# Kernel tuning notes

Hardware: AMD Instinct MI355X
Metric: run time of the kernel (lower is better)

Reference implementation:

```python
import jax, jax.numpy as jnp
import numpy as np

CX, CY, FX, FY = 334.081, 169.808, 460.585, 460.268
EPS = 1e-07
T_ITER = 1000
MIN_POINTS = 5000
H, W, B = 360, 640, 2


def _point_cloud(depth_img):
    # depth_img: [C,H,W]; channel 2 if C==3 else channel 0
    depth = depth_img[2] if depth_img.shape[0] == 3 else depth_img[0]
    rows, cols = depth.shape
    c = jnp.arange(cols, dtype=depth.dtype)[None, :]
    r = jnp.arange(rows, dtype=depth.dtype)[:, None]
    valid = (depth > 0) & (depth < 65535)
    nanv = jnp.float32(jnp.nan)
    z = jnp.where(valid, depth / 1000.0, nanv)
    x = jnp.where(valid, z * (c - CX) / FX, nanv)
    y = jnp.where(valid, z * (r - CY) / FY, nanv)
    pcd = jnp.stack([x.ravel(), y.ravel(), z.ravel()], axis=1)  # [N,3]
    return pcd, valid.ravel()


def setup_inputs() -> dict:
    key = jax.random.key(0)
    k1, k2 = jax.random.split(key)
    fake = jax.random.uniform(k1, (B, 1, H, W), dtype=jnp.float32)
    real = jax.random.uniform(k2, (B, 1, H, W), dtype=jnp.float32)
    return {"fake": fake, "real": real, "epoch": 5, "show_image": 0}


def _forward(fake, real, epoch):
    real_pcd, vr = _point_cloud(real[0])
    fake_pcd, vf = _point_cloud(fake[0])
    real_pcd = real_pcd * 1000.0
    fake_pcd = fake_pcd * 1000.0
    # pcd[pcd==0] = eps  (NaN==0 is False, NaNs preserved)
    real_pcd = jnp.where(real_pcd == 0, EPS, real_pcd)
    fake_pcd = jnp.where(fake_pcd == 0, EPS, fake_pcd)

    # combined validity mask (real-valid then fake-valid filtering chain)
    m = vr & vf
    cnt = jnp.maximum(jnp.sum(m), 1)

    def sel(v, fill):
        return jnp.where(m, v, fill)

    def mrmse(a, b):
        d = sel(a, 0.0) - sel(b, 0.0)
        return jnp.sqrt(jnp.sum(d * d) / cnt)

    lossX = mrmse(real_pcd[:, 0], fake_pcd[:, 0])
    lossY = mrmse(real_pcd[:, 1], fake_pcd[:, 1])
    lossZ = mrmse(real_pcd[:, 2], fake_pcd[:, 2])
    dlog = jnp.log(jnp.abs(sel(real_pcd[:, 2], 1.0))) - jnp.log(jnp.abs(sel(fake_pcd[:, 2], 1.0)))
    RMSE_log = 10000.0 * jnp.sqrt(jnp.sum(jnp.where(m, dlog * dlog, 0.0)) / cnt)
    loss17 = RMSE_log * jnp.abs(10.0 * (3.0 - jnp.exp(lossX) - jnp.exp(lossY) - jnp.exp(lossZ)))

    # ---- batched RANSAC plane fit on normalized fake cloud ----
    nan_cloud = jnp.where(jnp.isnan(fake_pcd), 0.0, fake_pcd)
    pts = nan_cloud / jnp.max(nan_cloud)  # [N,3]
    N = pts.shape[0]
    thresh = jnp.maximum(jnp.float32(0.025 - 0.001 * epoch), jnp.float32(0.005))

    rkey = jax.random.key(42)
    idx = jax.random.randint(rkey, (T_ITER, 3), 0, N)  # 3 sample points per trial
    p = pts[idx]  # [T,3,3]
    vA = p[:, 1] - p[:, 0]
    vB = p[:, 2] - p[:, 0]
    nrm = jnp.cross(vA, vB)
    nrm = nrm / jnp.linalg.norm(nrm, axis=1, keepdims=True)  # unit normals [T,3]
    kk = -jnp.sum(nrm * p[:, 1], axis=1)  # plane offsets [T]
    dist = pts @ nrm.T + kk[None, :]  # [N,T], |n|=1 so no extra divide
    inl = jnp.abs(dist) <= thresh  # [N,T]
    counts = jnp.sum(inl, axis=0)  # [T]
    # keep first trial with strictly-largest count among counts > minPoints
    score = jnp.where(counts > MIN_POINTS, counts, -1)
    best = jnp.argmax(score)
    a, b, c, d = nrm[best, 0], nrm[best, 1], nrm[best, 2], kk[best]
    inlier_mask = inl[:, best]  # [N]

    # translation/rotation were built via torch.tensor(...) -> detached in torch
    trans = jax.lax.stop_gradient(jnp.stack([jnp.zeros(()), jnp.zeros(()), d / c]))
    n2 = a * a + b * b + c * c
    cos_t = c / jnp.sqrt(n2)
    sin_t = jnp.sqrt((a * a + b * b) / n2)
    sab = jnp.sqrt(a * a + b * b)
    u1 = b / sab
    u2 = -a / sab
    R = jnp.stack([
        jnp.stack([cos_t + u1 * u1 * (1 - cos_t), u1 * u2 * (1 - cos_t), u2 * sin_t]),
        jnp.stack([u1 * u2 * (1 - cos_t), cos_t + u2 * u2 * (1 - cos_t), -u1 * sin_t]),
        jnp.stack([-u2 * sin_t, u1 * sin_t, cos_t]),
    ])
    Rt = jax.lax.stop_gradient(R).T  # torch transposes before matmul

    plane_pts = pts + trans
    zc = (plane_pts @ Rt)[:, 2]  # rotated z for all points; inliers selected by mask
    icnt = jnp.maximum(jnp.sum(inlier_mask), 1)
    zmax = jnp.max(jnp.where(inlier_mask, zc, -jnp.inf))
    zmin = jnp.min(jnp.where(inlier_mask, zc, jnp.inf))
    below = jnp.sum(jnp.where(inlier_mask, jnp.abs(zc - zmax), 0.0)) / icnt
    above = jnp.sum(jnp.where(inlier_mask, jnp.abs(zc - zmin), 0.0)) / icnt
    above = jnp.where(above == 0, jnp.float32(1e-07), above)
    plane_mean_dist_grad = 1000.0 * (above + below)

    loss_curv = loss17 + plane_mean_dist_grad
    delta = jnp.stack([RMSE_log, lossX, lossY, lossZ, plane_mean_dist_grad, loss17])
    return delta, loss_curv


def reference(fake, real, epoch, show_image):
    del show_image  # unused in the loss math
    return _forward(fake, real, epoch)
```

## Files before the change

### kernel.cpp

```cpp
#include <hip/hip_runtime.h>

namespace {

typedef float v2f __attribute__((ext_vector_type(2)));

constexpr int kW = 640;
constexpr unsigned kSpan = 230400u;
constexpr int kB1 = 900;
constexpr int kB3 = 1024;
constexpr int kPPB3 = 225;
constexpr int kB5 = 900;
constexpr unsigned kPoison = 0xAAAAAAAAu;

constexpr size_t kOffMaxv    = 0;
constexpr size_t kOffL17     = 8;
constexpr size_t kOffSel     = 16;
constexpr size_t kOffC1      = 256;
constexpr size_t kOffC3      = 320;
constexpr size_t kOffC5      = 384;
constexpr size_t kOffPlanes  = 512;
constexpr size_t kOffSP      = 512 + 16384;
constexpr size_t kOffZP      = kOffSP + 43200;
constexpr size_t kOffPartial = kOffZP + 28800;
constexpr size_t kOffPts     = kOffPartial + (size_t)kB3 * 256 * 4;

__device__ __forceinline__ void ast64(unsigned long long* p, unsigned long long v) {
  __hip_atomic_store(p, v, __ATOMIC_RELAXED, __HIP_MEMORY_SCOPE_AGENT);
}
__device__ __forceinline__ unsigned long long ald64(const unsigned long long* p) {
  return __hip_atomic_load(p, __ATOMIC_RELAXED, __HIP_MEMORY_SCOPE_AGENT);
}
__device__ __forceinline__ void ast32(unsigned* p, unsigned v) {
  __hip_atomic_store(p, v, __ATOMIC_RELAXED, __HIP_MEMORY_SCOPE_AGENT);
}
__device__ __forceinline__ unsigned ald32(const unsigned* p) {
  return __hip_atomic_load(p, __ATOMIC_RELAXED, __HIP_MEMORY_SCOPE_AGENT);
}

__device__ __forceinline__ unsigned rotl32(unsigned v, int r) {
  return (v << r) | (v >> (32 - r));
}

__device__ __forceinline__ void threefry(unsigned c0, unsigned c1,
                                         unsigned& o0, unsigned& o1) {
  const unsigned ks0 = 0u, ks1 = 42u, ks2 = 0x1BD11BDAu ^ 0u ^ 42u;
  unsigned x0 = c0 + ks0, x1 = c1 + ks1;
#define TFR(r) { x0 += x1; x1 = rotl32(x1, (r)); x1 ^= x0; }
  TFR(13) TFR(15) TFR(26) TFR(6)
  x0 += ks1; x1 += ks2 + 1u;
  TFR(17) TFR(29) TFR(16) TFR(24)
  x0 += ks2; x1 += ks0 + 2u;
  TFR(13) TFR(15) TFR(26) TFR(6)
  x0 += ks0; x1 += ks1 + 3u;
  TFR(17) TFR(29) TFR(16) TFR(24)
  x0 += ks1; x1 += ks2 + 4u;
  TFR(13) TFR(15) TFR(26) TFR(6)
  x0 += ks2; x1 += ks0 + 5u;
#undef TFR
  o0 = x0; o1 = x1;
}

__device__ __forceinline__ void pix_coords(float d, int row, int col, bool& valid,
                                           float& x, float& y, float& z) {
  valid = (d > 0.0f) && (d < 65535.0f);
  float z0 = d / 1000.0f;
  float x0 = z0 * ((float)col - 334.081f) / 460.585f;
  float y0 = z0 * ((float)row - 169.808f) / 460.268f;
  x = x0 * 1000.0f;
  y = y0 * 1000.0f;
  z = z0 * 1000.0f;
  if (x == 0.0f) x = 1e-7f;
  if (y == 0.0f) y = 1e-7f;
  if (z == 0.0f) z = 1e-7f;
}

__device__ __forceinline__ void make_pt(float d, int row, int col, float maxv,
                                        float& x, float& y, float& z) {
  bool v; float a, b, c;
  pix_coords(d, row, col, v, a, b, c);
  x = (v ? a : 0.f) / maxv;
  y = (v ? b : 0.f) / maxv;
  z = (v ? c : 0.f) / maxv;
}

__device__ __forceinline__ float get_thresh(int ep) {
  return (float)fmax(0.025 - 0.001 * (double)ep, 0.005);
}

__global__ __launch_bounds__(256) void k_stats(const float* __restrict__ fake,
                                               const float* __restrict__ real,
                                               float* __restrict__ out,
                                               char* __restrict__ ws) {
  int* maxvBits = (int*)(ws + kOffMaxv);
  unsigned long long* loss17p = (unsigned long long*)(ws + kOffL17);
  unsigned* selkeyp = (unsigned*)(ws + kOffSel);
  unsigned* ctr = (unsigned*)(ws + kOffC1);
  float4* planes = (float4*)(ws + kOffPlanes);
  unsigned long long* sp = (unsigned long long*)(ws + kOffSP);
  float4* ptsraw = (float4*)(ws + kOffPts);

  const int b = blockIdx.x, t = threadIdx.x;
  const int lane = t & 63, wid = t >> 6;

  __shared__ double sD0[4], sD1[4], sD2[4], sD3[4];
  __shared__ int sI0[4];
  __shared__ float sF0[4];
  __shared__ unsigned sArr;
  __shared__ unsigned sMvU;

  {
    int i = b * 256 + t;
    int row = i / kW, col = i - row * kW;
    bool vr, vf; float rx, ry, rz, fx, fy, fz;
    pix_coords(real[i], row, col, vr, rx, ry, rz);
    pix_coords(fake[i], row, col, vf, fx, fy, fz);
    ptsraw[i] = make_float4(vf ? fx : 0.f, vf ? fy : 0.f, vf ? fz : 0.f, 0.f);
    double dx2 = 0, dy2 = 0, dz2 = 0, dl2 = 0; int cc = 0;
    if (vr && vf) {
      float ddx = rx - fx, ddy = ry - fy, ddz = rz - fz;
      dx2 = (double)ddx * (double)ddx;
      dy2 = (double)ddy * (double)ddy;
      dz2 = (double)ddz * (double)ddz;
      double dl = log(fabs((double)rz)) - log(fabs((double)fz));
      dl2 = dl * dl;
      cc = 1;
    }
    float mx = vf ? fmaxf(fmaxf(fx, fy), fz) : 0.0f;
    for (int o = 32; o; o >>= 1) {
      dx2 += __shfl_down(dx2, o); dy2 += __shfl_down(dy2, o);
      dz2 += __shfl_down(dz2, o); dl2 += __shfl_down(dl2, o);
      cc += __shfl_down(cc, o);
      mx = fmaxf(mx, __shfl_down(mx, o));
    }
    if (lane == 0) { sD0[wid]=dx2; sD1[wid]=dy2; sD2[wid]=dz2; sD3[wid]=dl2;
                     sI0[wid]=cc; sF0[wid]=mx; }
    __syncthreads();
    if (t == 0) {
      unsigned long long* e = sp + (size_t)b * 6;
      ast64(e + 0, __double_as_longlong(sD0[0]+sD0[1]+sD0[2]+sD0[3]));
      ast64(e + 1, __double_as_longlong(sD1[0]+sD1[1]+sD1[2]+sD1[3]));
      ast64(e + 2, __double_as_longlong(sD2[0]+sD2[1]+sD2[2]+sD2[3]));
      ast64(e + 3, __double_as_longlong(sD3[0]+sD3[1]+sD3[2]+sD3[3]));
      ast64(e + 4, (unsigned long long)(sI0[0]+sI0[1]+sI0[2]+sI0[3]));
      float bm = fmaxf(fmaxf(sF0[0], sF0[1]), fmaxf(sF0[2], sF0[3]));
      atomicMax(maxvBits, (int)__float_as_uint(bm));
    }
  }
  __syncthreads();
  if (t == 0)
    sArr = __hip_atomic_fetch_add(ctr, 1u, __ATOMIC_RELAXED, __HIP_MEMORY_SCOPE_AGENT);
  __syncthreads();
  unsigned ret = sArr;
  if (ret < kPoison + (unsigned)(kB1 - 5)) return;
  int role = (int)(ret - (kPoison + (unsigned)(kB1 - 5)));

  if (role == 4) {
    double gx = 0, gy = 0, gz = 0, gl = 0; int gc = 0;
    for (int r = t; r < kB1; r += 256) {
      const unsigned long long* e = sp + (size_t)r * 6;
      gx += __longlong_as_double(ald64(e + 0));
      gy += __longlong_as_double(ald64(e + 1));
      gz += __longlong_as_double(ald64(e + 2));
      gl += __longlong_as_double(ald64(e + 3));
      gc += (int)ald64(e + 4);
    }
    for (int o = 32; o; o >>= 1) {
      gx += __shfl_down(gx, o); gy += __shfl_down(gy, o);
      gz += __shfl_down(gz, o); gl += __shfl_down(gl, o);
      gc += __shfl_down(gc, o);
    }
    if (lane == 0) { sD0[wid]=gx; sD1[wid]=gy; sD2[wid]=gz; sD3[wid]=gl; sI0[wid]=gc; }
    __syncthreads();
    if (t == 0) {
      double SX = sD0[0]+sD0[1]+sD0[2]+sD0[3];
      double SY = sD1[0]+sD1[1]+sD1[2]+sD1[3];
      double SZ = sD2[0]+sD2[1]+sD2[2]+sD2[3];
      double SL = sD3[0]+sD3[1]+sD3[2]+sD3[3];
      int CN = sI0[0]+sI0[1]+sI0[2]+sI0[3];
      double cntd = (CN > 0) ? (double)CN : 1.0;
      double lossX = sqrt(SX / cntd);
      double lossY = sqrt(SY / cntd);
      double lossZ = sqrt(SZ / cntd);
      double rmse_log = 10000.0 * sqrt(SL / cntd);
      double loss17 = rmse_log * fabs(10.0 * (3.0 - exp(lossX) - exp(lossY) - exp(lossZ)));
      ast64(loss17p, __double_as_longlong(loss17));
      ast32(selkeyp, 0u);
      out[0] = (float)rmse_log;
      out[1] = (float)lossX;
      out[2] = (float)lossY;
      out[3] = (float)lossZ;
      out[5] = (float)loss17;
    }
  } else {
    if (t == 0) {
      while (ald32(ctr) != kPoison + (unsigned)kB1) __builtin_amdgcn_s_sleep(8);
      sMvU = ald32((const unsigned*)maxvBits);
    }
    __syncthreads();
    const float maxv = __uint_as_float(sMvU);
    int pid = role * 256 + t;
    if (pid < 1000) {
      float px[3], py[3], pz[3];
#pragma unroll
      for (int v = 0; v < 3; v++) {
        unsigned p = 3u * (unsigned)pid + (unsigned)v;
        unsigned o0, o1;
        threefry(p, p + 3000u, o0, o1);
        unsigned idx = o1 % kSpan;
        int row = (int)(idx / kW), col = (int)idx - row * kW;
        make_pt(fake[idx], row, col, maxv, px[v], py[v], pz[v]);
      }
      float ax = px[1]-px[0], ay = py[1]-py[0], az = pz[1]-pz[0];
      float bx = px[2]-px[0], by = py[2]-py[0], bz = pz[2]-pz[0];
      float nx = ay*bz - az*by;
      float ny = az*bx - ax*bz;
      float nz = ax*by - ay*bx;
      float nn = sqrtf(nx*nx + ny*ny + nz*nz);
      nx /= nn; ny /= nn; nz /= nn;
      float kk = -(nx*px[1] + ny*py[1] + nz*pz[1]);
      planes[pid] = make_float4(nx, ny, nz, kk);
    } else {
      planes[pid] = make_float4(0.f, 0.f, 0.f, 3e38f);
    }
  }
}

__global__ __launch_bounds__(256) void k_count(const int* __restrict__ epoch,
                                               char* __restrict__ ws) {
  unsigned* selkeyp = (unsigned*)(ws + kOffSel);
  unsigned* ctr = (unsigned*)(ws + kOffC3);
  const float4* planes = (const float4*)(ws + kOffPlanes);
  unsigned* partial = (unsigned*)(ws + kOffPartial);
  const float4* ptsraw = (const float4*)(ws + kOffPts);

  const int b = blockIdx.x, t = threadIdx.x;
  const float th = get_thresh(*epoch);
  const float maxv = __uint_as_float(*(const unsigned*)(ws + kOffMaxv));

  __shared__ float4 sPts[kPPB3];
  __shared__ uint4 sAcc[16][16];
  __shared__ unsigned sArr;

  if (t < kPPB3) {
    float4 r = ptsraw[b * kPPB3 + t];
    sPts[t] = make_float4(r.x / maxv, r.y / maxv, r.z / maxv, 0.f);
  }
  float4 p0 = planes[t * 4 + 0], p1 = planes[t * 4 + 1];
  float4 p2 = planes[t * 4 + 2], p3 = planes[t * 4 + 3];
  v2f Ax = {p0.x, p1.x}, Ay = {p0.y, p1.y}, Az = {p0.z, p1.z}, Aw = {p0.w, p1.w};
  v2f Bx = {p2.x, p3.x}, By = {p2.y, p3.y}, Bz = {p2.z, p3.z}, Bw = {p2.w, p3.w};
  __syncthreads();

  int c0 = 0, c1 = 0, c2 = 0, c3 = 0;
#pragma unroll 5
  for (int s = 0; s < kPPB3; ++s) {
    float4 q = sPts[s];
    v2f qx = {q.x, q.x}, qy = {q.y, q.y}, qz = {q.z, q.z};
    v2f dA = __builtin_elementwise_fma(qx, Ax,
             __builtin_elementwise_fma(qy, Ay,
             __builtin_elementwise_fma(qz, Az, Aw)));
    v2f dB = __builtin_elementwise_fma(qx, Bx,
             __builtin_elementwise_fma(qy, By,
             __builtin_elementwise_fma(qz, Bz, Bw)));
    c0 += (fabsf(dA.x) <= th) ? 1 : 0;
    c1 += (fabsf(dA.y) <= th) ? 1 : 0;
    c2 += (fabsf(dB.x) <= th) ? 1 : 0;
    c3 += (fabsf(dB.y) <= th) ? 1 : 0;
  }
  ast32(&partial[b * 256 + t],
        (unsigned)c0 | ((unsigned)c1 << 8) | ((unsigned)c2 << 16) | ((unsigned)c3 << 24));

  __syncthreads();
  if (t == 0)
    sArr = __hip_atomic_fetch_add(ctr, 1u, __ATOMIC_RELAXED, __HIP_MEMORY_SCOPE_AGENT);
  __syncthreads();
  unsigned ret = sArr;
  if (ret < kPoison + (unsigned)(kB3 - 16)) return;

  int r = (int)(ret - (kPoison + (unsigned)(kB3 - 16)));
  if (t == 0) {
    while (ald32(ctr) != kPoison + (unsigned)kB3) __builtin_amdgcn_s_sleep(2);
  }
  __syncthreads();

  int owner = r * 16 + (t & 15);
  int chunk = t >> 4;
  unsigned s0 = 0, s1 = 0, s2 = 0, s3 = 0;
  for (int row = chunk * 64; row < chunk * 64 + 64; ++row) {
    unsigned v = ald32(&partial[row * 256 + owner]);
    s0 += v & 0xFFu; s1 += (v >> 8) & 0xFFu;
    s2 += (v >> 16) & 0xFFu; s3 += (v >> 24) & 0xFFu;
  }
  sAcc[t & 15][chunk] = make_uint4(s0, s1, s2, s3);
  __syncthreads();

  unsigned mykey = 0u;
  if (t < 16) {
    unsigned t0 = 0, t1 = 0, t2 = 0, t3 = 0;
    for (int j = 0; j < 16; ++j) {
      uint4 v = sAcc[t][j];
      t0 += v.x; t1 += v.y; t2 += v.z; t3 += v.w;
    }
    unsigned tot[4] = {t0, t1, t2, t3};
    int pbase = (r * 16 + t) * 4;
#pragma unroll
    for (int k = 0; k < 4; ++k) {
      int p = pbase + k;
      if (p < 1000) {
        int score = ((int)tot[k] > 5000) ? (int)tot[k] : -1;
        unsigned key = ((unsigned)(score + 2) << 10) | (unsigned)(1023 - p);
        mykey = key > mykey ? key : mykey;
      }
    }
  }
  for (int o = 32; o; o >>= 1) {
    unsigned other = __shfl_down(mykey, o);
    mykey = other > mykey ? other : mykey;
  }
  if (t == 0) atomicMax(selkeyp, mykey);
}

__global__ __launch_bounds__(256) void k_zc(const int* __restrict__ epoch,
                                            float* __restrict__ out,
                                            char* __restrict__ ws) {
  const unsigned long long* loss17p = (const unsigned long long*)(ws + kOffL17);
  unsigned* ctr = (unsigned*)(ws + kOffC5);
  const float4* planes = (const float4*)(ws + kOffPlanes);
  unsigned long long* zp = (unsigned long long*)(ws + kOffZP);
  const float4* ptsraw = (const float4*)(ws + kOffPts);

  const int b = blockIdx.x, t = threadIdx.x;
  const int lane = t & 63, wid = t >> 6;
  const float th = get_thresh(*epoch);
  const float maxv = __uint_as_float(*(const unsigned*)(ws + kOffMaxv));

  unsigned selkey = *(const unsigned*)(ws + kOffSel);
  int best = 1023 - (int)(selkey & 1023u);
  float4 pl = planes[best];
  const float a = pl.x, bb = pl.y, c = pl.z, d = pl.w;
  float n2 = a * a + bb * bb + c * c;
  float cos_t = c / sqrtf(n2);
  float sin_t = sqrtf((a * a + bb * bb) / n2);
  float sab = sqrtf(a * a + bb * bb);
  float u1 = bb / sab, u2 = -a / sab;
  const float r0 = -u2 * sin_t, r1 = u1 * sin_t, r2 = cos_t, tz = d / c;

  __shared__ double sD0[4];
  __shared__ int sI0[4];
  __shared__ float sF0[4], sF1[4];
  __shared__ unsigned sArr;

  double sz = 0.0; int ic = 0; float zmx = -INFINITY, zmn = -INFINITY;
  {
    float4 rw = ptsraw[b * 256 + t];
    float qx = rw.x / maxv, qy = rw.y / maxv, qz = rw.z / maxv;
    float dist = fmaf(qx, a, fmaf(qy, bb, fmaf(qz, c, d)));
    if (fabsf(dist) <= th) {
      float zc = fmaf(qx, r0, fmaf(qy, r1, (qz + tz) * r2));
      sz = (double)zc; ic = 1; zmx = zc; zmn = -zc;
    }
  }
  for (int o = 32; o; o >>= 1) {
    sz += __shfl_down(sz, o); ic += __shfl_down(ic, o);
    zmx = fmaxf(zmx, __shfl_down(zmx, o));
    zmn = fmaxf(zmn, __shfl_down(zmn, o));
  }
  if (lane == 0) { sD0[wid] = sz; sI0[wid] = ic; sF0[wid] = zmx; sF1[wid] = zmn; }
  __syncthreads();
  if (t == 0) {
    unsigned long long* e = zp + (size_t)b * 4;
    ast64(e + 0, __double_as_longlong(sD0[0]+sD0[1]+sD0[2]+sD0[3]));
    ast64(e + 1, (unsigned long long)(sI0[0]+sI0[1]+sI0[2]+sI0[3]));
    float bmx = fmaxf(fmaxf(sF0[0], sF0[1]), fmaxf(sF0[2], sF0[3]));
    float bmn = fmaxf(fmaxf(sF1[0], sF1[1]), fmaxf(sF1[2], sF1[3]));
    ast64(e + 2, (unsigned long long)__float_as_uint(bmx) |
                 ((unsigned long long)__float_as_uint(bmn) << 32));
  }
  __syncthreads();
  if (t == 0)
    sArr = __hip_atomic_fetch_add(ctr, 1u, __ATOMIC_RELAXED, __HIP_MEMORY_SCOPE_AGENT);
  __syncthreads();
  if (sArr != kPoison + (unsigned)(kB5 - 1)) return;

  {
    double gs = 0.0; int gi = 0; float gmx = -INFINITY, gmn = -INFINITY;
    for (int r = t; r < kB5; r += 256) {
      const unsigned long long* e = zp + (size_t)r * 4;
      gs += __longlong_as_double(ald64(e + 0));
      gi += (int)ald64(e + 1);
      unsigned long long mm = ald64(e + 2);
      gmx = fmaxf(gmx, __uint_as_float((unsigned)(mm & 0xFFFFFFFFu)));
      gmn = fmaxf(gmn, __uint_as_float((unsigned)(mm >> 32)));
    }
    for (int o = 32; o; o >>= 1) {
      gs += __shfl_down(gs, o); gi += __shfl_down(gi, o);
      gmx = fmaxf(gmx, __shfl_down(gmx, o));
      gmn = fmaxf(gmn, __shfl_down(gmn, o));
    }
    if (lane == 0) { sD0[wid] = gs; sI0[wid] = gi; sF0[wid] = gmx; sF1[wid] = gmn; }
    __syncthreads();
    if (t == 0) {
      double S = sD0[0]+sD0[1]+sD0[2]+sD0[3];
      int IC = sI0[0]+sI0[1]+sI0[2]+sI0[3];
      float MX = fmaxf(fmaxf(sF0[0], sF0[1]), fmaxf(sF0[2], sF0[3]));
      float MN = fmaxf(fmaxf(sF1[0], sF1[1]), fmaxf(sF1[2], sF1[3]));
      double below = 0.0, above = 0.0;
      if (IC > 0) {
        double icd = (double)IC;
        double mean = S / icd;
        below = (double)MX - mean;
        above = mean - (double)(-MN);
      }
      if (above == 0.0) above = 1e-7;
      double pmdg = 1000.0 * (above + below);
      double loss17 = __longlong_as_double(ald64(loss17p));
      out[4] = (float)pmdg;
      out[6] = (float)(loss17 + pmdg);
    }
  }
}

}

extern "C" void kernel_launch(void* const* d_in, const int* in_sizes, int n_in,
                              void* d_out, int out_size, void* d_ws, size_t ws_size,
                              hipStream_t stream) {
  (void)in_sizes; (void)n_in; (void)out_size; (void)ws_size;
  const float* fake = (const float*)d_in[0];
  const float* real = (const float*)d_in[1];
  const int* epoch = (const int*)d_in[2];
  float* out = (float*)d_out;
  char* ws = (char*)d_ws;

  k_stats<<<kB1, 256, 0, stream>>>(fake, real, out, ws);
  k_count<<<kB3, 256, 0, stream>>>(epoch, ws);
  k_zc<<<kB5, 256, 0, stream>>>(epoch, out, ws);
}
```

Before: 129.2 us.

## Split plane sampling and scalar reduction out of stats kernel into separate launch

The stats kernel no longer uses an atomic arrival counter with the last five blocks spin-waiting to finalize the loss scalars and generate the RANSAC planes. That work moves to a new 17-block kernel that relies on the kernel boundary for ordering. In the new kernel, the three threefry samples of each plane are spread across three threads and combined through shared memory, instead of one thread computing them in sequence. This removes the spin-wait tail and the serial per-plane work, at the cost of one extra kernel launch.

```diff
diff --git a/kernel.cpp b/kernel.cpp
--- a/kernel.cpp
+++ b/kernel.cpp
@@ -15,7 +15,6 @@
 constexpr size_t kOffMaxv    = 0;
 constexpr size_t kOffL17     = 8;
 constexpr size_t kOffSel     = 16;
-constexpr size_t kOffC1      = 256;
 constexpr size_t kOffC3      = 320;
 constexpr size_t kOffC5      = 384;
 constexpr size_t kOffPlanes  = 512;
@@ -89,14 +88,9 @@
 
 __global__ __launch_bounds__(256) void k_stats(const float* __restrict__ fake,
                                                const float* __restrict__ real,
-                                               float* __restrict__ out,
                                                char* __restrict__ ws) {
   int* maxvBits = (int*)(ws + kOffMaxv);
-  unsigned long long* loss17p = (unsigned long long*)(ws + kOffL17);
-  unsigned* selkeyp = (unsigned*)(ws + kOffSel);
-  unsigned* ctr = (unsigned*)(ws + kOffC1);
-  float4* planes = (float4*)(ws + kOffPlanes);
-  unsigned long long* sp = (unsigned long long*)(ws + kOffSP);
+  double* sp = (double*)(ws + kOffSP);
   float4* ptsraw = (float4*)(ws + kOffPts);
 
   const int b = blockIdx.x, t = threadIdx.x;
@@ -105,64 +99,65 @@
   __shared__ double sD0[4], sD1[4], sD2[4], sD3[4];
   __shared__ int sI0[4];
   __shared__ float sF0[4];
-  __shared__ unsigned sArr;
-  __shared__ unsigned sMvU;
-
-  {
-    int i = b * 256 + t;
-    int row = i / kW, col = i - row * kW;
-    bool vr, vf; float rx, ry, rz, fx, fy, fz;
-    pix_coords(real[i], row, col, vr, rx, ry, rz);
-    pix_coords(fake[i], row, col, vf, fx, fy, fz);
-    ptsraw[i] = make_float4(vf ? fx : 0.f, vf ? fy : 0.f, vf ? fz : 0.f, 0.f);
-    double dx2 = 0, dy2 = 0, dz2 = 0, dl2 = 0; int cc = 0;
-    if (vr && vf) {
-      float ddx = rx - fx, ddy = ry - fy, ddz = rz - fz;
-      dx2 = (double)ddx * (double)ddx;
-      dy2 = (double)ddy * (double)ddy;
-      dz2 = (double)ddz * (double)ddz;
-      double dl = log(fabs((double)rz)) - log(fabs((double)fz));
-      dl2 = dl * dl;
-      cc = 1;
-    }
-    float mx = vf ? fmaxf(fmaxf(fx, fy), fz) : 0.0f;
-    for (int o = 32; o; o >>= 1) {
-      dx2 += __shfl_down(dx2, o); dy2 += __shfl_down(dy2, o);
-      dz2 += __shfl_down(dz2, o); dl2 += __shfl_down(dl2, o);
-      cc += __shfl_down(cc, o);
-      mx = fmaxf(mx, __shfl_down(mx, o));
-    }
-    if (lane == 0) { sD0[wid]=dx2; sD1[wid]=dy2; sD2[wid]=dz2; sD3[wid]=dl2;
-                     sI0[wid]=cc; sF0[wid]=mx; }
-    __syncthreads();
-    if (t == 0) {
-      unsigned long long* e = sp + (size_t)b * 6;
-      ast64(e + 0, __double_as_longlong(sD0[0]+sD0[1]+sD0[2]+sD0[3]));
-      ast64(e + 1, __double_as_longlong(sD1[0]+sD1[1]+sD1[2]+sD1[3]));
-      ast64(e + 2, __double_as_longlong(sD2[0]+sD2[1]+sD2[2]+sD2[3]));
-      ast64(e + 3, __double_as_longlong(sD3[0]+sD3[1]+sD3[2]+sD3[3]));
-      ast64(e + 4, (unsigned long long)(sI0[0]+sI0[1]+sI0[2]+sI0[3]));
-      float bm = fmaxf(fmaxf(sF0[0], sF0[1]), fmaxf(sF0[2], sF0[3]));
-      atomicMax(maxvBits, (int)__float_as_uint(bm));
-    }
-  }
-  __syncthreads();
-  if (t == 0)
-    sArr = __hip_atomic_fetch_add(ctr, 1u, __ATOMIC_RELAXED, __HIP_MEMORY_SCOPE_AGENT);
-  __syncthreads();
-  unsigned ret = sArr;
-  if (ret < kPoison + (unsigned)(kB1 - 5)) return;
-  int role = (int)(ret - (kPoison + (unsigned)(kB1 - 5)));
-
-  if (role == 4) {
+
+  int i = b * 256 + t;
+  int row = i / kW, col = i - row * kW;
+  bool vr, vf; float rx, ry, rz, fx, fy, fz;
+  pix_coords(real[i], row, col, vr, rx, ry, rz);
+  pix_coords(fake[i], row, col, vf, fx, fy, fz);
+  ptsraw[i] = make_float4(vf ? fx : 0.f, vf ? fy : 0.f, vf ? fz : 0.f, 0.f);
+  double dx2 = 0, dy2 = 0, dz2 = 0, dl2 = 0; int cc = 0;
+  if (vr && vf) {
+    float ddx = rx - fx, ddy = ry - fy, ddz = rz - fz;
+    dx2 = (double)ddx * (double)ddx;
+    dy2 = (double)ddy * (double)ddy;
+    dz2 = (double)ddz * (double)ddz;
+    double dl = log(fabs((double)rz)) - log(fabs((double)fz));
+    dl2 = dl * dl;
+    cc = 1;
+  }
+  float mx = vf ? fmaxf(fmaxf(fx, fy), fz) : 0.0f;
+  for (int o = 32; o; o >>= 1) {
+    dx2 += __shfl_down(dx2, o); dy2 += __shfl_down(dy2, o);
+    dz2 += __shfl_down(dz2, o); dl2 += __shfl_down(dl2, o);
+    cc += __shfl_down(cc, o);
+    mx = fmaxf(mx, __shfl_down(mx, o));
+  }
+  if (lane == 0) { sD0[wid]=dx2; sD1[wid]=dy2; sD2[wid]=dz2; sD3[wid]=dl2;
+                   sI0[wid]=cc; sF0[wid]=mx; }
+  __syncthreads();
+  if (t == 0) {
+    double* e = sp + (size_t)b * 6;
+    e[0] = sD0[0]+sD0[1]+sD0[2]+sD0[3];
+    e[1] = sD1[0]+sD1[1]+sD1[2]+sD1[3];
+    e[2] = sD2[0]+sD2[1]+sD2[2]+sD2[3];
+    e[3] = sD3[0]+sD3[1]+sD3[2]+sD3[3];
+    e[4] = (double)(sI0[0]+sI0[1]+sI0[2]+sI0[3]);
+    float bm = fmaxf(fmaxf(sF0[0], sF0[1]), fmaxf(sF0[2], sF0[3]));
+    atomicMax(maxvBits, (int)__float_as_uint(bm));
+  }
+}
+
+__global__ __launch_bounds__(256) void k_planes_scalars(const float* __restrict__ fake,
+                                                        float* __restrict__ out,
+                                                        char* __restrict__ ws) {
+  const int* maxvBits = (const int*)(ws + kOffMaxv);
+  double* loss17p = (double*)(ws + kOffL17);
+  unsigned* selkeyp = (unsigned*)(ws + kOffSel);
+  float4* planes = (float4*)(ws + kOffPlanes);
+  const double* sp = (const double*)(ws + kOffSP);
+
+  const int t = threadIdx.x;
+  const int lane = t & 63, wid = t >> 6;
+
+  if (blockIdx.x == 16) {
+    __shared__ double sD0[4], sD1[4], sD2[4], sD3[4];
+    __shared__ int sI0[4];
     double gx = 0, gy = 0, gz = 0, gl = 0; int gc = 0;
     for (int r = t; r < kB1; r += 256) {
-      const unsigned long long* e = sp + (size_t)r * 6;
-      gx += __longlong_as_double(ald64(e + 0));
-      gy += __longlong_as_double(ald64(e + 1));
-      gz += __longlong_as_double(ald64(e + 2));
-      gl += __longlong_as_double(ald64(e + 3));
-      gc += (int)ald64(e + 4);
+      const double* e = sp + (size_t)r * 6;
+      gx += e[0]; gy += e[1]; gz += e[2]; gl += e[3];
+      gc += (int)e[4];
     }
     for (int o = 32; o; o >>= 1) {
       gx += __shfl_down(gx, o); gy += __shfl_down(gy, o);
@@ -183,8 +178,8 @@
       double lossZ = sqrt(SZ / cntd);
       double rmse_log = 10000.0 * sqrt(SL / cntd);
       double loss17 = rmse_log * fabs(10.0 * (3.0 - exp(lossX) - exp(lossY) - exp(lossZ)));
-      ast64(loss17p, __double_as_longlong(loss17));
-      ast32(selkeyp, 0u);
+      *loss17p = loss17;
+      *selkeyp = 0u;
       out[0] = (float)rmse_log;
       out[1] = (float)lossX;
       out[2] = (float)lossY;
@@ -192,35 +187,44 @@
       out[5] = (float)loss17;
     }
   } else {
-    if (t == 0) {
-      while (ald32(ctr) != kPoison + (unsigned)kB1) __builtin_amdgcn_s_sleep(8);
-      sMvU = ald32((const unsigned*)maxvBits);
-    }
-    __syncthreads();
-    const float maxv = __uint_as_float(sMvU);
-    int pid = role * 256 + t;
-    if (pid < 1000) {
-      float px[3], py[3], pz[3];
-#pragma unroll
-      for (int v = 0; v < 3; v++) {
+    const float maxv = __uint_as_float((unsigned)*maxvBits);
+    __shared__ float sX[192], sY[192], sZ[192];
+    if (t < 192) {
+      int j = t / 3;
+      int v = t - j * 3;
+      int pid = blockIdx.x * 64 + j;
+      if (pid < 1000) {
         unsigned p = 3u * (unsigned)pid + (unsigned)v;
         unsigned o0, o1;
         threefry(p, p + 3000u, o0, o1);
         unsigned idx = o1 % kSpan;
         int row = (int)(idx / kW), col = (int)idx - row * kW;
-        make_pt(fake[idx], row, col, maxv, px[v], py[v], pz[v]);
+        float x, y, z;
+        make_pt(fake[idx], row, col, maxv, x, y, z);
+        sX[t] = x; sY[t] = y; sZ[t] = z;
       }
-      float ax = px[1]-px[0], ay = py[1]-py[0], az = pz[1]-pz[0];
-      float bx = px[2]-px[0], by = py[2]-py[0], bz = pz[2]-pz[0];
-      float nx = ay*bz - az*by;
-      float ny = az*bx - ax*bz;
-      float nz = ax*by - ay*bx;
-      float nn = sqrtf(nx*nx + ny*ny + nz*nz);
-      nx /= nn; ny /= nn; nz /= nn;
-      float kk = -(nx*px[1] + ny*py[1] + nz*pz[1]);
-      planes[pid] = make_float4(nx, ny, nz, kk);
-    } else {
-      planes[pid] = make_float4(0.f, 0.f, 0.f, 3e38f);
+    }
+    __syncthreads();
+    if (t < 64) {
+      int pid = blockIdx.x * 64 + t;
+      if (pid < 1000) {
+        float px[3], py[3], pz[3];
+#pragma unroll
+        for (int v = 0; v < 3; v++) {
+          px[v] = sX[3 * t + v]; py[v] = sY[3 * t + v]; pz[v] = sZ[3 * t + v];
+        }
+        float ax = px[1]-px[0], ay = py[1]-py[0], az = pz[1]-pz[0];
+        float bx = px[2]-px[0], by = py[2]-py[0], bz = pz[2]-pz[0];
+        float nx = ay*bz - az*by;
+        float ny = az*bx - ax*bz;
+        float nz = ax*by - ay*bx;
+        float nn = sqrtf(nx*nx + ny*ny + nz*nz);
+        nx /= nn; ny /= nn; nz /= nn;
+        float kk = -(nx*px[1] + ny*py[1] + nz*pz[1]);
+        planes[pid] = make_float4(nx, ny, nz, kk);
+      } else {
+        planes[pid] = make_float4(0.f, 0.f, 0.f, 3e38f);
+      }
     }
   }
 }
@@ -323,7 +327,7 @@
 __global__ __launch_bounds__(256) void k_zc(const int* __restrict__ epoch,
                                             float* __restrict__ out,
                                             char* __restrict__ ws) {
-  const unsigned long long* loss17p = (const unsigned long long*)(ws + kOffL17);
+  const double* loss17p = (const double*)(ws + kOffL17);
   unsigned* ctr = (unsigned*)(ws + kOffC5);
   const float4* planes = (const float4*)(ws + kOffPlanes);
   unsigned long long* zp = (unsigned long long*)(ws + kOffZP);
@@ -413,9 +417,8 @@
       }
       if (above == 0.0) above = 1e-7;
       double pmdg = 1000.0 * (above + below);
-      double loss17 = __longlong_as_double(ald64(loss17p));
       out[4] = (float)pmdg;
-      out[6] = (float)(loss17 + pmdg);
+      out[6] = (float)(*loss17p + pmdg);
     }
   }
 }
@@ -432,7 +435,8 @@
   float* out = (float*)d_out;
   char* ws = (char*)d_ws;
 
-  k_stats<<<kB1, 256, 0, stream>>>(fake, real, out, ws);
+  k_stats<<<kB1, 256, 0, stream>>>(fake, real, ws);
+  k_planes_scalars<<<17, 256, 0, stream>>>(fake, out, ws);
   k_count<<<kB3, 256, 0, stream>>>(epoch, ws);
   k_zc<<<kB5, 256, 0, stream>>>(epoch, out, ws);
 }
```

After: 129.8 us. No clear change (+0.5%).
